# Optimization experiments

Measured on AMD Instinct MI355X. Metric: run time of the kernel, lower is better.

The kernel has to match this reference:

```python
import jax, jax.numpy as jnp
import numpy as np

DVEC = 128
B, S = 4, 1024


def setup_inputs() -> dict:
    key = jax.random.key(0)
    k1, k2 = jax.random.split(key)
    func_and_arg = jax.random.normal(k1, (B, S, 2 * DVEC), dtype=jnp.float32)
    cooccurrences = jax.random.normal(k2, (DVEC, DVEC, DVEC), dtype=jnp.float32)
    return {"func_and_arg": func_and_arg, "cooccurrences": cooccurrences}


def reference(func_and_arg, cooccurrences):
    # out[b,s,z] = sum_{i,j} func[b,s,i] * cooc[i,j,z] * arg[b,s,j]
    d = cooccurrences.shape[0]
    func = func_and_arg[..., :d]   # [B,S,D]
    arg = func_and_arg[..., d:]    # [B,S,D]
    # contract func over i first -> [B,S,D(j),Z], then arg over j -> [B,S,Z]
    tmp = jnp.einsum('bsi,ijz->bsjz', func, cooccurrences)
    return jnp.einsum('bsjz,bsj->bsz', tmp, arg)
```

## Files before the change

kernel.cpp:

```cpp
#include <hip/hip_runtime.h>
#include <hip/hip_bf16.h>


typedef __attribute__((ext_vector_type(8))) short bf16x8;
typedef __attribute__((ext_vector_type(4))) float f32x4;

__device__ __forceinline__ unsigned pkbf16(float x, float y) {
    __hip_bfloat162 h = __float22bfloat162_rn(make_float2(x, y));
    unsigned u; __builtin_memcpy(&u, &h, sizeof(u));
    return u;
}

template<int USE_WS>
__global__ __launch_bounds__(512, 1) void cooc_main(
    const float* __restrict__ fa, const float* __restrict__ Cc,
    float* __restrict__ dst)
{
    __shared__ __align__(16) ushort bT[2][64 * 136];

    const int bid   = blockIdx.x;
    const int mtile = bid >> 4;
    const int kp = bid & 7;
    const int zp = (bid >> 3) & 1;
    const int t0 = mtile * 256;
    const int i0 = kp * 16;
    const int z0 = zp * 64;

    const int tid  = threadIdx.x;
    const int lane = tid & 63;
    const int wv = tid >> 6;
    const int mg = wv >> 1;
    const int zg = wv & 1;
    const int lm = lane & 15;
    const int lk = lane >> 4;

    union { unsigned u[4]; bf16x8 v; } a_pk[4][4];
    #pragma unroll
    for (int m = 0; m < 4; ++m) {
        const float* ab = fa + (size_t)(t0 + mg * 64 + m * 16 + lm) * 256 + 128;
        #pragma unroll
        for (int ks = 0; ks < 4; ++ks) {
            float4 q0 = *(const float4*)(ab + ks * 32 + lk * 8);
            float4 q1 = *(const float4*)(ab + ks * 32 + lk * 8 + 4);
            a_pk[m][ks].u[0] = pkbf16(q0.x, q0.y);
            a_pk[m][ks].u[1] = pkbf16(q0.z, q0.w);
            a_pk[m][ks].u[2] = pkbf16(q1.x, q1.y);
            a_pk[m][ks].u[3] = pkbf16(q1.z, q1.w);
        }
    }

    const int zq = tid & 15;
    const int jq = tid >> 4;
    const float* csrc = Cc + (size_t)i0 * 16384 + (size_t)(jq * 4) * 128 + z0 + zq * 4;
    union { float4 v4[4]; float f[16]; } La;

    auto loads = [&](int s) {
        const float* p = csrc + (size_t)s * 16384;
        #pragma unroll
        for (int r = 0; r < 4; ++r) La.v4[r] = *(const float4*)(p + r * 128);
    };
    auto writes = [&](int b) {
        const int pos = ((jq >> 1) + zq) & 15;
        #pragma unroll
        for (int rr = 0; rr < 4; ++rr) {
            const int zl = zq * 4 + rr;
            const unsigned lo = pkbf16(La.f[0 * 4 + rr], La.f[1 * 4 + rr]);
            const unsigned hi = pkbf16(La.f[2 * 4 + rr], La.f[3 * 4 + rr]);
            *(uint2*)&bT[b][zl * 136 + pos * 8 + (jq & 1) * 4] = make_uint2(lo, hi);
        }
    };

    loads(0); writes(0);
    __syncthreads();

    float acc[4][2][4];
    #pragma unroll
    for (int m = 0; m < 4; ++m)
        #pragma unroll
        for (int n = 0; n < 2; ++n)
            #pragma unroll
            for (int r = 0; r < 4; ++r) acc[m][n][r] = 0.f;

    const float* fptr = fa + (size_t)(t0 + mg * 64 + lk * 4) * 256 + i0;

    #pragma unroll 2
    for (int s = 0; s < 16; ++s) {
        const int p = s & 1;

        float fv[4][4];
        #pragma unroll
        for (int m = 0; m < 4; ++m)
            #pragma unroll
            for (int r = 0; r < 4; ++r)
                fv[m][r] = fptr[(size_t)(m * 16 + r) * 256 + s];

        if (s < 15) loads(s + 1);

        bf16x8 Bf[4][2];
        #pragma unroll
        for (int ks = 0; ks < 4; ++ks)
            #pragma unroll
            for (int n = 0; n < 2; ++n) {
                const int zz = zg * 32 + n * 16 + lm;
                const int pos = ((ks * 4 + lk) + (zz >> 2)) & 15;
                Bf[ks][n] = *(const bf16x8*)&bT[p][zz * 136 + pos * 8];
            }

        #pragma unroll
        for (int m = 0; m < 4; ++m)
            #pragma unroll
            for (int n = 0; n < 2; ++n) {
                f32x4 g = {0.f, 0.f, 0.f, 0.f};
                #pragma unroll
                for (int ks = 0; ks < 4; ++ks)
                    g = __builtin_amdgcn_mfma_f32_16x16x32_bf16(a_pk[m][ks].v, Bf[ks][n], g, 0, 0, 0);
                #pragma unroll
                for (int r = 0; r < 4; ++r)
                    acc[m][n][r] += fv[m][r] * g[r];
            }

        if (s < 15) writes(p ^ 1);
        __syncthreads();
    }

    #pragma unroll
    for (int m = 0; m < 4; ++m)
        #pragma unroll
        for (int n = 0; n < 2; ++n)
            #pragma unroll
            for (int r = 0; r < 4; ++r) {
                const int row = t0 + mg * 64 + m * 16 + lk * 4 + r;
                const int col = z0 + zg * 32 + n * 16 + lm;
                if (USE_WS)
                    dst[(size_t)kp * 524288 + (size_t)row * 128 + col] = acc[m][n][r];
                else
                    atomicAdd(&dst[(size_t)row * 128 + col], acc[m][n][r]);
            }
}

__global__ __launch_bounds__(256) void cooc_reduce(const float* __restrict__ ws,
                                                   float* __restrict__ out) {
    const size_t idx = ((size_t)blockIdx.x * 256 + threadIdx.x) * 4;
    float4 a = *(const float4*)(ws + idx);
    #pragma unroll
    for (int k = 1; k < 8; ++k) {
        float4 b = *(const float4*)(ws + (size_t)k * 524288 + idx);
        a.x += b.x; a.y += b.y; a.z += b.z; a.w += b.w;
    }
    *(float4*)(out + idx) = a;
}

extern "C" void kernel_launch(void* const* d_in, const int* in_sizes, int n_in,
                              void* d_out, int out_size, void* d_ws, size_t ws_size,
                              hipStream_t stream) {
    const float* fa = (const float*)d_in[0];
    const float* Cc = (const float*)d_in[1];
    float* out = (float*)d_out;

    const bool use_ws = ws_size >= (size_t)8 * 524288 * sizeof(float);
    if (use_ws) {
        cooc_main<1><<<256, 512, 0, stream>>>(fa, Cc, (float*)d_ws);
        cooc_reduce<<<512, 256, 0, stream>>>((const float*)d_ws, out);
    } else {
        (void)hipMemsetAsync(out, 0, (size_t)out_size * sizeof(float), stream);
        cooc_main<0><<<256, 512, 0, stream>>>(fa, Cc, out);
    }
}
```

Baseline: 95.47 us.

## Halve block size to 256 threads, stage func scalars in LDS

Blocks now cover 128 tokens with 256 threads, launched as 512 blocks with two blocks per CU, so each thread loads twice as many cooccurrence rows per stage. The per-step func scalars are preloaded once into a transposed LDS array and read as float4, replacing the strided scalar global loads in the inner loop. The next-stage prefetch is moved ahead of the LDS reads. The aims are better occupancy, less per-step global latency, and a smaller tail from more blocks, at the cost of more registers per thread and more LDS per block.

```diff
diff --git a/kernel.cpp b/kernel.cpp
--- a/kernel.cpp
+++ b/kernel.cpp
@@ -12,17 +12,18 @@
 }
 
 template<int USE_WS>
-__global__ __launch_bounds__(512, 1) void cooc_main(
+__global__ __launch_bounds__(256, 2) void cooc_main(
     const float* __restrict__ fa, const float* __restrict__ Cc,
     float* __restrict__ dst)
 {
     __shared__ __align__(16) ushort bT[2][64 * 136];
+    __shared__ float f_lds[16][128];
 
     const int bid   = blockIdx.x;
+    const int kp    = bid & 7;
+    const int zp    = (bid >> 3) & 1;
     const int mtile = bid >> 4;
-    const int kp = bid & 7;
-    const int zp = (bid >> 3) & 1;
-    const int t0 = mtile * 256;
+    const int t0 = mtile * 128;
     const int i0 = kp * 16;
     const int z0 = zp * 64;
 
@@ -33,6 +34,18 @@
     const int zg = wv & 1;
     const int lm = lane & 15;
     const int lk = lane >> 4;
+
+    {
+        const int row = tid & 127;
+        const int sh = (tid >> 7) * 8;
+        const float* fp = fa + (size_t)(t0 + row) * 256 + i0 + sh;
+        float4 v0 = *(const float4*)fp;
+        float4 v1 = *(const float4*)(fp + 4);
+        f_lds[sh + 0][row] = v0.x; f_lds[sh + 1][row] = v0.y;
+        f_lds[sh + 2][row] = v0.z; f_lds[sh + 3][row] = v0.w;
+        f_lds[sh + 4][row] = v1.x; f_lds[sh + 5][row] = v1.y;
+        f_lds[sh + 6][row] = v1.z; f_lds[sh + 7][row] = v1.w;
+    }
 
     union { unsigned u[4]; bf16x8 v; } a_pk[4][4];
     #pragma unroll
@@ -49,24 +62,33 @@
         }
     }
 
-    const int zq = tid & 15;
-    const int jq = tid >> 4;
-    const float* csrc = Cc + (size_t)i0 * 16384 + (size_t)(jq * 4) * 128 + z0 + zq * 4;
-    union { float4 v4[4]; float f[16]; } La;
+    const int zq  = tid & 15;
+    const int jq0 = tid >> 4;
+    const float* csrc0 = Cc + (size_t)i0 * 16384 + (size_t)(jq0 * 4) * 128 + z0 + zq * 4;
+    const float* csrc1 = csrc0 + 16 * 4 * 128;
+    union { float4 v4[4]; float f[16]; } La[2];
 
     auto loads = [&](int s) {
-        const float* p = csrc + (size_t)s * 16384;
+        const float* p0 = csrc0 + (size_t)s * 16384;
+        const float* p1 = csrc1 + (size_t)s * 16384;
         #pragma unroll
-        for (int r = 0; r < 4; ++r) La.v4[r] = *(const float4*)(p + r * 128);
+        for (int r = 0; r < 4; ++r) {
+            La[0].v4[r] = *(const float4*)(p0 + r * 128);
+            La[1].v4[r] = *(const float4*)(p1 + r * 128);
+        }
     };
     auto writes = [&](int b) {
-        const int pos = ((jq >> 1) + zq) & 15;
         #pragma unroll
-        for (int rr = 0; rr < 4; ++rr) {
-            const int zl = zq * 4 + rr;
-            const unsigned lo = pkbf16(La.f[0 * 4 + rr], La.f[1 * 4 + rr]);
-            const unsigned hi = pkbf16(La.f[2 * 4 + rr], La.f[3 * 4 + rr]);
-            *(uint2*)&bT[b][zl * 136 + pos * 8 + (jq & 1) * 4] = make_uint2(lo, hi);
+        for (int part = 0; part < 2; ++part) {
+            const int jq = jq0 + part * 16;
+            const int pos = ((jq >> 1) + zq) & 15;
+            #pragma unroll
+            for (int rr = 0; rr < 4; ++rr) {
+                const int zl = zq * 4 + rr;
+                const unsigned lo = pkbf16(La[part].f[0 * 4 + rr], La[part].f[1 * 4 + rr]);
+                const unsigned hi = pkbf16(La[part].f[2 * 4 + rr], La[part].f[3 * 4 + rr]);
+                *(uint2*)&bT[b][zl * 136 + pos * 8 + (jq & 1) * 4] = make_uint2(lo, hi);
+            }
         }
     };
 
@@ -81,20 +103,15 @@
             #pragma unroll
             for (int r = 0; r < 4; ++r) acc[m][n][r] = 0.f;
 
-    const float* fptr = fa + (size_t)(t0 + mg * 64 + lk * 4) * 256 + i0;
-
     #pragma unroll 2
     for (int s = 0; s < 16; ++s) {
         const int p = s & 1;
+        if (s < 15) loads(s + 1);
 
-        float fv[4][4];
+        float4 f4[4];
         #pragma unroll
         for (int m = 0; m < 4; ++m)
-            #pragma unroll
-            for (int r = 0; r < 4; ++r)
-                fv[m][r] = fptr[(size_t)(m * 16 + r) * 256 + s];
-
-        if (s < 15) loads(s + 1);
+            f4[m] = *(const float4*)&f_lds[s][mg * 64 + m * 16 + lk * 4];
 
         bf16x8 Bf[4][2];
         #pragma unroll
@@ -114,9 +131,10 @@
                 #pragma unroll
                 for (int ks = 0; ks < 4; ++ks)
                     g = __builtin_amdgcn_mfma_f32_16x16x32_bf16(a_pk[m][ks].v, Bf[ks][n], g, 0, 0, 0);
-                #pragma unroll
-                for (int r = 0; r < 4; ++r)
-                    acc[m][n][r] += fv[m][r] * g[r];
+                acc[m][n][0] += f4[m].x * g[0];
+                acc[m][n][1] += f4[m].y * g[1];
+                acc[m][n][2] += f4[m].z * g[2];
+                acc[m][n][3] += f4[m].w * g[3];
             }
 
         if (s < 15) writes(p ^ 1);
@@ -159,10 +177,10 @@
 
     const bool use_ws = ws_size >= (size_t)8 * 524288 * sizeof(float);
     if (use_ws) {
-        cooc_main<1><<<256, 512, 0, stream>>>(fa, Cc, (float*)d_ws);
+        cooc_main<1><<<512, 256, 0, stream>>>(fa, Cc, (float*)d_ws);
         cooc_reduce<<<512, 256, 0, stream>>>((const float*)d_ws, out);
     } else {
         (void)hipMemsetAsync(out, 0, (size_t)out_size * sizeof(float), stream);
-        cooc_main<0><<<256, 512, 0, stream>>>(fa, Cc, out);
+        cooc_main<0><<<512, 256, 0, stream>>>(fa, Cc, out);
     }
 }
```

After: 92.06 us. 1.04x faster.
